# Performance work log

Measured on AMD Instinct MI355X. Metric: run time of the kernel, lower is better.

Reference implementation:

```python
import jax, jax.numpy as jnp
import numpy as np

N_NODES = 100000
N_EDGES = 3200000
D = 256
L = 3
BN_EPS = 1e-5


def setup_inputs() -> dict:
    key = jax.random.key(0)
    ks = jax.random.split(key, 6)
    scale = 1.0 / np.sqrt(D)
    x = jax.random.normal(ks[0], (N_NODES, D), dtype=jnp.float32)
    W = jax.random.normal(ks[1], (L, D, D), dtype=jnp.float32) * scale
    b = jnp.zeros((L, D), dtype=jnp.float32)
    Wl = jax.random.normal(ks[2], (L, D, D), dtype=jnp.float32) * scale
    bl = jnp.zeros((L, D), dtype=jnp.float32)
    gamma = jnp.ones((L, D), dtype=jnp.float32)
    beta = jnp.zeros((L, D), dtype=jnp.float32)
    src = jax.random.randint(ks[3], (N_EDGES,), 0, N_NODES, dtype=jnp.int32)
    dst = jax.random.randint(ks[4], (N_EDGES,), 0, N_NODES, dtype=jnp.int32)
    return {"x": x, "W": W, "b": b, "Wl": Wl, "bl": bl,
            "gamma": gamma, "beta": beta, "src": src, "dst": dst}


def _gcn_head(x, W, b, Wl, bl, gamma, beta, src, dst):
    n = x.shape[0]
    ones = jnp.ones((src.shape[0],), dtype=x.dtype)
    # degrees (clamped to 1, as DGL GraphConv does)
    deg_out = jnp.maximum(jax.ops.segment_sum(ones, src, num_segments=n), 1.0)
    deg_in = jnp.maximum(jax.ops.segment_sum(ones, dst, num_segments=n), 1.0)
    inv_sqrt_out = (deg_out ** -0.5)[:, None]  # [N,1]
    inv_sqrt_in = (deg_in ** -0.5)[:, None]

    h = x
    for l in range(W.shape[0]):
        # GraphConv, norm='both': D_in^{-1/2} A D_out^{-1/2} h W + b
        hs = h * inv_sqrt_out
        agg = jax.ops.segment_sum(hs[src], dst, num_segments=n)  # [N,D]
        agg = agg * inv_sqrt_in
        out = agg @ W[l] + b[l]
        # residual + optional linear on the layer input
        out = out + h + (h @ Wl[l] + bl[l])
        # BatchNorm1d over nodes (training-style batch stats, biased var)
        mean = jnp.mean(out, axis=0)
        var = jnp.var(out, axis=0)
        out = gamma[l] * (out - mean) * jax.lax.rsqrt(var + BN_EPS) + beta[l]
        # ReLU (Dropout treated as identity / eval mode)
        h = jax.nn.relu(out)
    return h


def reference(x, W, b, Wl, bl, gamma, beta, src, dst):
    return _gcn_head(x, W, b, Wl, bl, gamma, beta, src, dst)
```

## Files before the change

kernel.cpp:

```cpp
#include <hip/hip_runtime.h>

#define D 256
#define BN_EPS 1e-5f

typedef __attribute__((ext_vector_type(8))) short short8;
typedef __attribute__((ext_vector_type(4))) float f32x4;
typedef __attribute__((ext_vector_type(2))) float f32x2;

__device__ __forceinline__ float b2f(ushort u) {
    union { unsigned u; float f; } c; c.u = ((unsigned)u) << 16; return c.f;
}
__device__ __forceinline__ ushort f2b(float f) {
    union { float f; unsigned u; } c; c.f = f;
    return (ushort)((c.u + 0x7fffu + ((c.u >> 16) & 1u)) >> 16);
}

typedef __attribute__((address_space(1))) const void gv_t;
typedef __attribute__((address_space(3))) void lv_t;
__device__ __forceinline__ void gld16(const void* g, void* l) {
    __builtin_amdgcn_global_load_lds((gv_t*)g, (lv_t*)l, 16, 0, 0);
}

__device__ __forceinline__ uint2 pk_fp8x8(const float* r) {
    unsigned w0 = 0, w1 = 0;
    w0 = __builtin_amdgcn_cvt_pk_fp8_f32(r[0], r[1], w0, false);
    w0 = __builtin_amdgcn_cvt_pk_fp8_f32(r[2], r[3], w0, true);
    w1 = __builtin_amdgcn_cvt_pk_fp8_f32(r[4], r[5], w1, false);
    w1 = __builtin_amdgcn_cvt_pk_fp8_f32(r[6], r[7], w1, true);
    return make_uint2(w0, w1);
}


#define HB 64

__global__ __launch_bounds__(256) void hist_kernel(const int* __restrict__ src,
                                                   const int* __restrict__ dst,
                                                   unsigned* __restrict__ P, int E) {
    __shared__ unsigned lhist[16384];
    int combo = blockIdx.y;
    const int* arr = (combo >> 2) ? dst : src;
    unsigned base = (unsigned)(combo & 3) << 15;
    for (int j = threadIdx.x; j < 16384; j += 256) lhist[j] = 0;
    __syncthreads();
    int i0 = (blockIdx.x * 256 + threadIdx.x) * 4;
    int stride = HB * 256 * 4;
    for (int i = i0; i < E; i += stride) {
        if (i + 3 < E) {
            int4 v = *(const int4*)(arr + i);
            unsigned r0 = (unsigned)v.x - base;
            unsigned r1 = (unsigned)v.y - base;
            unsigned r2 = (unsigned)v.z - base;
            unsigned r3 = (unsigned)v.w - base;
            if (r0 < 32768u) atomicAdd(&lhist[r0 >> 1], 1u << ((r0 & 1) << 4));
            if (r1 < 32768u) atomicAdd(&lhist[r1 >> 1], 1u << ((r1 & 1) << 4));
            if (r2 < 32768u) atomicAdd(&lhist[r2 >> 1], 1u << ((r2 & 1) << 4));
            if (r3 < 32768u) atomicAdd(&lhist[r3 >> 1], 1u << ((r3 & 1) << 4));
        } else {
            for (int j = i; j < E; j++) {
                unsigned r = (unsigned)arr[j] - base;
                if (r < 32768u) atomicAdd(&lhist[r >> 1], 1u << ((r & 1) << 4));
            }
        }
    }
    __syncthreads();
    unsigned* dstp = P + ((size_t)(combo * HB + blockIdx.x) << 14);
    for (int j = threadIdx.x; j < 16384; j += 256) dstp[j] = lhist[j];
}

__global__ void histreduce_kernel(const unsigned* __restrict__ P,
                                  int* __restrict__ cntO, int* __restrict__ cntI, int N) {
    int g = blockIdx.x * 256 + threadIdx.x;
    int array = g >> 16;
    int p = g & 65535;
    int range = p >> 14;
    int j = p & 16383;
    const unsigned* Pp = P + ((size_t)((array * 4 + range) * HB) << 14) + j;
    unsigned s = 0;
#pragma unroll 8
    for (int b = 0; b < HB; b++) s += Pp[(size_t)b << 14];
    int bin = (range << 15) + 2 * j;
    int* cnt = array ? cntI : cntO;
    if (bin < N)     cnt[bin]     = (int)(s & 0xFFFFu);
    if (bin + 1 < N) cnt[bin + 1] = (int)(s >> 16);
}

__global__ void invsqrt_kernel(const int* __restrict__ cntO, const int* __restrict__ cntI,
                               float* __restrict__ invO, float* __restrict__ invOI,
                               float* __restrict__ sqrtO, int N) {
    int i = blockIdx.x * blockDim.x + threadIdx.x;
    if (i < N) {
        float dO = (float)max(cntO[i], 1);
        float io = rsqrtf(dO);
        invO[i] = io;
        sqrtO[i] = sqrtf(dO);
        invOI[i] = io * rsqrtf((float)max(cntI[i], 1));
    }
}

__global__ void scan1_kernel(const int* __restrict__ cnt, int* __restrict__ off,
                             int* __restrict__ bsum, int n) {
    __shared__ int s[256];
    int t = threadIdx.x;
    int i0 = blockIdx.x * 1024 + t * 4;
    int v0 = (i0 < n) ? ((cnt[i0] + 7) & ~7) : 0;
    int v1 = (i0 + 1 < n) ? ((cnt[i0 + 1] + 7) & ~7) : 0;
    int v2 = (i0 + 2 < n) ? ((cnt[i0 + 2] + 7) & ~7) : 0;
    int v3 = (i0 + 3 < n) ? ((cnt[i0 + 3] + 7) & ~7) : 0;
    int tsum = v0 + v1 + v2 + v3;
    s[t] = tsum;
    __syncthreads();
    for (int d = 1; d < 256; d <<= 1) {
        int x = (t >= d) ? s[t - d] : 0;
        __syncthreads();
        s[t] += x;
        __syncthreads();
    }
    int excl = s[t] - tsum;
    if (i0 < n)     off[i0]     = excl;
    if (i0 + 1 < n) off[i0 + 1] = excl + v0;
    if (i0 + 2 < n) off[i0 + 2] = excl + v0 + v1;
    if (i0 + 3 < n) off[i0 + 3] = excl + v0 + v1 + v2;
    if (t == 255) bsum[blockIdx.x] = s[255];
}

__global__ void scan2_kernel(int* __restrict__ bsum, int nb) {
    __shared__ int s[256];
    int t = threadIdx.x;
    int v = (t < nb) ? bsum[t] : 0;
    s[t] = v;
    __syncthreads();
    for (int d = 1; d < 256; d <<= 1) {
        int x = (t >= d) ? s[t - d] : 0;
        __syncthreads();
        s[t] += x;
        __syncthreads();
    }
    if (t < nb) bsum[t] = s[t] - v;
    if (t == nb - 1) bsum[1023] = s[t];
}

__global__ void scan3_kernel(int* __restrict__ off, const int* __restrict__ bsum,
                             int* __restrict__ bucketCur, int n) {
    int i = blockIdx.x * blockDim.x + threadIdx.x;
    if (i < n) {
        int v = off[i] + bsum[i >> 10];
        off[i] = v;
        if ((i & 255) == 0) bucketCur[i >> 8] = v;
    } else if (i == n) {
        off[n] = bsum[1023];
    }
}


#define NBKMAX 512

__global__ __launch_bounds__(256) void partA_kernel(const int* __restrict__ src,
                                                    const int* __restrict__ dst,
                                                    int* __restrict__ bucketCur,
                                                    unsigned* __restrict__ pairs,
                                                    int E, int NBK) {
    __shared__ int cnt[NBKMAX];
    __shared__ int base_s[NBKMAX];
    for (int j = threadIdx.x; j < NBK; j += 256) cnt[j] = 0;
    __syncthreads();
    for (int i = blockIdx.x * 256 + threadIdx.x; i < E; i += gridDim.x * 256)
        atomicAdd(&cnt[((unsigned)dst[i]) >> 8], 1);
    __syncthreads();
    for (int j = threadIdx.x; j < NBK; j += 256) {
        base_s[j] = atomicAdd(&bucketCur[j], cnt[j]);
        cnt[j] = 0;
    }
    __syncthreads();
    for (int i = blockIdx.x * 256 + threadIdx.x; i < E; i += gridDim.x * 256) {
        unsigned d = (unsigned)dst[i];
        unsigned b = d >> 8;
        int pos = base_s[b] + atomicAdd(&cnt[b], 1);
        pairs[pos] = ((unsigned)src[i] << 8) | (d & 255u);
    }
}

#define BCAP 14336

__global__ __launch_bounds__(256) void partB_kernel(const unsigned* __restrict__ pairs,
                                                    const int* __restrict__ off,
                                                    const int* __restrict__ bucketCur,
                                                    int* __restrict__ srcS, int N) {
    __shared__ int curL[256];
    __shared__ int stage[BCAP];
    int b = blockIdx.x;
    int n0 = b << 8;
    int n1 = min(n0 + 256, N);
    int base = off[n0];
    int len = off[n1] - base;
    if (len > BCAP) len = BCAP;
    for (int j = threadIdx.x; j < len; j += 256) stage[j] = N;
    int nn = n1 - n0;
    for (int i = threadIdx.x; i < nn; i += 256) curL[i] = off[n0 + i] - base;
    __syncthreads();
    int cntB = bucketCur[b] - base;
    for (int j = threadIdx.x; j < cntB; j += 256) {
        unsigned p = pairs[base + j];
        int pos = atomicAdd(&curL[p & 255u], 1);
        if (pos < BCAP) stage[pos] = (int)(p >> 8);
    }
    __syncthreads();
    for (int j4 = threadIdx.x; j4 * 4 < len; j4 += 256)
        *(int4*)(srcS + base + j4 * 4) = *(const int4*)(stage + j4 * 4);
}

__global__ void init_pad_kernel(ushort* __restrict__ X, unsigned* __restrict__ X8,
                                int N, long strideH) {
    int t = threadIdx.x;
    X[(size_t)N * D + t] = 0;
    if (t < 64) X8[(t >> 5) * strideH + (size_t)N * 32 + (t & 31)] = 0;
}


__global__ void prep_w_kernel(const float* __restrict__ W, const float* __restrict__ Wl,
                              const float* __restrict__ b, const float* __restrict__ bl,
                              ushort* __restrict__ Wt, float* __restrict__ bcat, int L) {
    int idx = blockIdx.x * blockDim.x + threadIdx.x;
    int k = idx & 511;
    int n = (idx >> 9) & 255;
    int l = idx >> 17;
    if (l >= L) return;
    float v;
    if (k < 256) {
        v = W[(size_t)l * 65536 + k * 256 + n];
    } else {
        v = Wl[(size_t)l * 65536 + (k - 256) * 256 + n];
        if (k - 256 == n) v += 1.0f;
    }
    Wt[idx] = f2b(v);
    if (k == 0) bcat[l * 256 + n] = b[l * 256 + n] + bl[l * 256 + n];
}

__global__ void x2b_kernel(const float* __restrict__ x, const float* __restrict__ invO,
                           ushort* __restrict__ hs, unsigned* __restrict__ hs8,
                           long strideH, long n8) {
    long i8 = (long)blockIdx.x * blockDim.x + threadIdx.x;
    if (i8 >= n8) return;
    long row = i8 >> 5;
    float sc = invO[row];
    float4 a = ((const float4*)x)[i8 * 2];
    float4 b = ((const float4*)x)[i8 * 2 + 1];
    float r[8] = { a.x * sc, a.y * sc, a.z * sc, a.w * sc,
                   b.x * sc, b.y * sc, b.z * sc, b.w * sc };
    ushort v[8];
#pragma unroll
    for (int j = 0; j < 8; j++) v[j] = f2b(r[j]);
    *(short8*)(hs + i8 * 8) = *(short8*)v;
    long H = (i8 >> 4) & 1;
    *(uint2*)(hs8 + H * strideH + row * 32 + (i8 & 15) * 2) = pk_fp8x8(r);
}


__global__ void aggregate_kernel(const unsigned* __restrict__ hs8h,
                                 const float* __restrict__ invOI,
                                 const int* __restrict__ off, const int* __restrict__ srcS,
                                 ushort* __restrict__ aggsh, int N) {
    int tid = threadIdx.x;
    int wid = tid >> 6, lane = tid & 63;
    int l32 = lane & 31;
    int node = blockIdx.x * 8 + wid * 2 + (lane >> 5);
    if (blockIdx.x * 8 + wid * 2 >= N) return;
    bool valid = node < N;
    int e0 = valid ? off[node] : 0;
    int e1 = valid ? off[node + 1] : 0;
    f32x2 A01 = {0.f, 0.f}, A23 = {0.f, 0.f};
    for (int e = e0; e < e1; e += 8) {
        int4 c0 = *(const int4*)(srcS + e);
        int4 c1 = *(const int4*)(srcS + e + 4);
        unsigned g0 = hs8h[(size_t)c0.x * 32 + l32];
        unsigned g1 = hs8h[(size_t)c0.y * 32 + l32];
        unsigned g2 = hs8h[(size_t)c0.z * 32 + l32];
        unsigned g3 = hs8h[(size_t)c0.w * 32 + l32];
        unsigned g4 = hs8h[(size_t)c1.x * 32 + l32];
        unsigned g5 = hs8h[(size_t)c1.y * 32 + l32];
        unsigned g6 = hs8h[(size_t)c1.z * 32 + l32];
        unsigned g7 = hs8h[(size_t)c1.w * 32 + l32];
#pragma unroll
        for (int q = 0; q < 8; q++) {
            unsigned g = (q == 0) ? g0 : (q == 1) ? g1 : (q == 2) ? g2 : (q == 3) ? g3
                       : (q == 4) ? g4 : (q == 5) ? g5 : (q == 6) ? g6 : g7;
            A01 += __builtin_amdgcn_cvt_pk_f32_fp8(g, false);
            A23 += __builtin_amdgcn_cvt_pk_f32_fp8(g, true);
        }
    }
    if (valid) {
        float wi = invOI[node];
        ushort4 o;
        o.x = f2b(A01[0] * wi); o.y = f2b(A01[1] * wi);
        o.z = f2b(A23[0] * wi); o.w = f2b(A23[1] * wi);
        *(ushort4*)(aggsh + (size_t)node * D + l32 * 4) = o;
    }
}


#define ASOFF(buf) ((buf) * 4096)
#define BSOFF(buf) (8192 + (buf) * 8192)

__global__ __launch_bounds__(512) void gemm_kernel(
        const ushort* __restrict__ aggs, const ushort* __restrict__ hs,
        const ushort* __restrict__ Wt,  const float* __restrict__ bcat,
        const float* __restrict__ sqrtO,
        ushort* __restrict__ tmp, float* __restrict__ bnsum, float* __restrict__ bnsq,
        int M) {
    __shared__ short SH[24576];

    int bm0 = blockIdx.x * 128;
    if (bm0 >= M) return;

    int tid = threadIdx.x;
    int wid = tid >> 6, lane = tid & 63;
    int wr = wid >> 2, wc = wid & 3;
    int lrow = lane & 15, lkh = lane >> 4;
    int srow = lane >> 2;
    int sseg = (lane & 3) ^ ((srow >> 1) & 3);

    f32x4 acc[4][4] = {};

#define STAGE(buf, k0s)                                                                    \
    {                                                                                      \
        int kk_ = (k0s) & 255;                                                             \
        const ushort* Ah_ = ((k0s) < 256) ? aggs : hs;                                     \
        gld16(Ah_ + (size_t)(bm0 + wid * 16 + srow) * 256 + kk_ + sseg * 8,                \
              SH + ASOFF(buf) + (wid * 16) * 32);                                          \
        const ushort* gb_ = Wt + (size_t)(wid * 32 + srow) * 512 + (k0s) + sseg * 8;       \
        gld16(gb_,            SH + BSOFF(buf) + (wid * 32) * 32);                          \
        gld16(gb_ + 16 * 512, SH + BSOFF(buf) + (wid * 32 + 16) * 32);                     \
    }

    STAGE(0, 0);

#pragma unroll
    for (int k0 = 0; k0 < 512; k0 += 32) {
        int cur = (k0 >> 5) & 1;
        __syncthreads();
        if (k0 + 32 < 512) STAGE(cur ^ 1, k0 + 32);

        short8 a[4], bfr[4];
#pragma unroll
        for (int m = 0; m < 4; m++) {
            int ra = wr * 64 + m * 16 + lrow;
            a[m] = *(short8*)&SH[ASOFF(cur) + ra * 32 + (lkh ^ ((ra >> 1) & 3)) * 8];
        }
#pragma unroll
        for (int n = 0; n < 4; n++) {
            int rb = wc * 64 + n * 16 + lrow;
            bfr[n] = *(short8*)&SH[BSOFF(cur) + rb * 32 + (lkh ^ ((rb >> 1) & 3)) * 8];
        }
#pragma unroll
        for (int m = 0; m < 4; m++)
#pragma unroll
            for (int n = 0; n < 4; n++)
                acc[m][n] = __builtin_amdgcn_mfma_f32_16x16x32_bf16(a[m], bfr[n], acc[m][n], 0, 0, 0);
    }
#undef STAGE

    ushort outv[4][4][4];
#pragma unroll
    for (int n = 0; n < 4; n++) {
        int col = wc * 64 + n * 16 + lrow;
        float bc = bcat[col];
        float s_part = 0.f, q_part = 0.f;
#pragma unroll
        for (int m = 0; m < 4; m++) {
            int rbase = bm0 + wr * 64 + m * 16 + lkh * 4;
#pragma unroll
            for (int i = 0; i < 4; i++) {
                int row = rbase + i;
                float v = (row < M) ? (acc[m][n][i] * sqrtO[row] + bc) : 0.f;
                outv[m][n][i] = f2b(v);
                if (row < M) { s_part += v; q_part += v * v; }
            }
        }
        s_part += __shfl_xor(s_part, 16);
        s_part += __shfl_xor(s_part, 32);
        q_part += __shfl_xor(q_part, 16);
        q_part += __shfl_xor(q_part, 32);
        if (lkh == 0) {
            atomicAdd(&bnsum[col], s_part);
            atomicAdd(&bnsq[col], q_part);
        }
    }

    for (int half = 0; half < 2; half++) {
        __syncthreads();
        if (wr == half) {
#pragma unroll
            for (int m = 0; m < 4; m++)
#pragma unroll
                for (int n = 0; n < 4; n++)
#pragma unroll
                    for (int i = 0; i < 4; i++)
                        SH[(m * 16 + lkh * 4 + i) * 256 + wc * 64 + n * 16 + lrow] =
                            (short)outv[m][n][i];
        }
        __syncthreads();
#pragma unroll
        for (int p = 0; p < 4; p++) {
            int rl = (tid >> 5) + p * 16;
            int row = bm0 + half * 64 + rl;
            if (row < M)
                *(short8*)(tmp + (size_t)row * 256 + (tid & 31) * 8) =
                    *(short8*)&SH[rl * 256 + (tid & 31) * 8];
        }
    }
}


__global__ void bnfin_kernel(float* __restrict__ bnsum, float* __restrict__ bnsq,
                             const float* __restrict__ gamma, const float* __restrict__ beta,
                             float2* __restrict__ bnab, float invM) {
    int c = threadIdx.x;
    float mean = bnsum[c] * invM;
    float var = bnsq[c] * invM - mean * mean;
    float a = gamma[c] * rsqrtf(var + BN_EPS);
    bnab[c] = make_float2(a, beta[c] - a * mean);
    bnsum[c] = 0.f;
    bnsq[c] = 0.f;
}

__global__ void bnrelu_kernel(const ushort* __restrict__ tmp, const float2* __restrict__ bnab,
                              const float* __restrict__ invO, ushort* __restrict__ Xout,
                              unsigned* __restrict__ X8out, long strideH,
                              float* __restrict__ out, int M, int last) {
    long i8 = (long)blockIdx.x * blockDim.x + threadIdx.x;
    if (i8 >= (long)M * 32) return;
    long row = i8 >> 5;
    int c0 = ((int)(i8 & 31)) * 8;
    short8 v = *(const short8*)(tmp + row * D + c0);
    float r[8];
#pragma unroll
    for (int j = 0; j < 8; j++) {
        float2 ab = bnab[c0 + j];
        float x = b2f((ushort)v[j]);
        r[j] = fmaxf(ab.x * x + ab.y, 0.f);
    }
    if (last) {
        float4 f0 = make_float4(r[0], r[1], r[2], r[3]);
        float4 f1 = make_float4(r[4], r[5], r[6], r[7]);
        ((float4*)(out + row * D + c0))[0] = f0;
        ((float4*)(out + row * D + c0))[1] = f1;
    } else {
        float sc = invO[row];
        ushort w[8];
#pragma unroll
        for (int j = 0; j < 8; j++) { r[j] *= sc; w[j] = f2b(r[j]); }
        *(short8*)(Xout + row * D + c0) = *(short8*)w;
        long H = (i8 >> 4) & 1;
        *(uint2*)(X8out + H * strideH + row * 32 + (i8 & 15) * 2) = pk_fp8x8(r);
    }
}


extern "C" void kernel_launch(void* const* d_in, const int* in_sizes, int n_in,
                              void* d_out, int out_size, void* d_ws, size_t ws_size,
                              hipStream_t stream) {
    const float* x     = (const float*)d_in[0];
    const float* W     = (const float*)d_in[1];
    const float* b     = (const float*)d_in[2];
    const float* Wl    = (const float*)d_in[3];
    const float* bl    = (const float*)d_in[4];
    const float* gamma = (const float*)d_in[5];
    const float* beta  = (const float*)d_in[6];
    const int*   src   = (const int*)d_in[7];
    const int*   dst   = (const int*)d_in[8];

    const int N = in_sizes[0] / D;
    const int E = in_sizes[7];
    const int L = in_sizes[1] / (D * D);
    const int M_pad = (N + 1 + 127) & ~127;
    const int E_pad = E + 7 * N + 64;
    const int NBK = (N + 255) >> 8;
    const long strideH = (long)M_pad * 32;
    float* out = (float*)d_out;

    char* p = (char*)d_ws;
    auto alloc = [&](size_t bytes) -> char* {
        char* r = p;
        p += (bytes + 255) & ~(size_t)255;
        return r;
    };
    int*      cur   = (int*)alloc((size_t)NBKMAX * 4);
    int*      cntO  = (int*)alloc((size_t)N * 4);
    int*      cntI  = (int*)alloc((size_t)N * 4);
    float*    invO  = (float*)alloc((size_t)(N + 1) * 4);
    float*    invOI = (float*)alloc((size_t)(N + 1) * 4);
    float*    sqrtO = (float*)alloc((size_t)(N + 1) * 4);
    int*      off_  = (int*)alloc((size_t)(N + 1) * 4);
    int*      bsum  = (int*)alloc(1024 * 4);
    int*      srcS  = (int*)alloc((size_t)E_pad * 4);
    ushort*   Wt    = (ushort*)alloc((size_t)L * 256 * 512 * 2);
    float*    bcat  = (float*)alloc((size_t)L * 256 * 4);
    ushort*   X     = (ushort*)alloc((size_t)M_pad * D * 2);
    unsigned* X8    = (unsigned*)alloc((size_t)2 * strideH * 4);
    ushort*   aggs  = (ushort*)alloc((size_t)M_pad * D * 2);
    ushort*   tmp   = (ushort*)alloc((size_t)M_pad * D * 2);
    float*    bnsum = (float*)alloc((size_t)2 * D * 4);
    float*    bnsq  = bnsum + D;
    float2*   bnab  = (float2*)alloc((size_t)D * 8);

    unsigned* P     = (unsigned*)aggs;
    unsigned* pairs = (unsigned*)aggs;

    {
        dim3 hg(HB, 8);
        hist_kernel<<<hg, 256, 0, stream>>>(src, dst, P, E);
        histreduce_kernel<<<512, 256, 0, stream>>>(P, cntO, cntI, N);
    }
    invsqrt_kernel<<<(N + 255) / 256, 256, 0, stream>>>(cntO, cntI, invO, invOI, sqrtO, N);
    int NB = (N + 1023) / 1024;
    scan1_kernel<<<NB, 256, 0, stream>>>(cntI, off_, bsum, N);
    scan2_kernel<<<1, 256, 0, stream>>>(bsum, NB);
    scan3_kernel<<<(N + 256) / 256, 256, 0, stream>>>(off_, bsum, cur, N);
    partA_kernel<<<512, 256, 0, stream>>>(src, dst, cur, pairs, E, NBK);
    partB_kernel<<<NBK, 256, 0, stream>>>(pairs, off_, cur, srcS, N);
    init_pad_kernel<<<1, 256, 0, stream>>>(X, X8, N, strideH);

    prep_w_kernel<<<(L * 256 * 512 + 255) / 256, 256, 0, stream>>>(W, Wl, b, bl, Wt, bcat, L);
    x2b_kernel<<<(int)(((long)N * 32 + 255) / 256), 256, 0, stream>>>(
        x, invO, X, X8, strideH, (long)N * 32);
    hipMemsetAsync(bnsum, 0, 2 * D * sizeof(float), stream);

    const int MB = (N + 127) / 128;
    const int agg_grid = (N + 7) / 8;
    const float invM = 1.0f / (float)N;
    for (int l = 0; l < L; l++) {
        int last = (l == L - 1);

        aggregate_kernel<<<agg_grid, 256, 0, stream>>>(X8, invOI, off_, srcS, aggs, N);
        aggregate_kernel<<<agg_grid, 256, 0, stream>>>(X8 + strideH, invOI, off_, srcS,
                                                       aggs + 128, N);

        gemm_kernel<<<MB, 512, 0, stream>>>(aggs, X, Wt + (size_t)l * 256 * 512,
                                            bcat + l * 256, sqrtO, tmp, bnsum, bnsq, N);

        bnfin_kernel<<<1, 256, 0, stream>>>(bnsum, bnsq, gamma + l * D, beta + l * D, bnab, invM);
        bnrelu_kernel<<<(int)(((long)N * 32 + 255) / 256), 256, 0, stream>>>(
            tmp, bnab, invO, X, X8, strideH, out, N, last);
    }
}
```

Baseline: 764.5 us.

## Single-buffer GEMM LDS to raise occupancy; merge aggregate halves into one launch

The GEMM drops its double-buffered LDS staging for a single buffer, which halves shared memory, and adds a launch-bounds hint so more blocks can be resident per CU. The epilogue now writes its output tile through LDS in four 32-row passes so it fits the smaller buffer. The two per-half aggregate launches become one 2D-grid launch that uses blockIdx.y to pick the half. The trade-off is that load/compute overlap inside a block is lost and each k-step needs an extra barrier, with the hope that higher occupancy hides the latency instead.

```diff
diff --git a/kernel.cpp b/kernel.cpp
--- a/kernel.cpp
+++ b/kernel.cpp
@@ -255,10 +255,12 @@
 }
 
 
-__global__ void aggregate_kernel(const unsigned* __restrict__ hs8h,
+__global__ void aggregate_kernel(const unsigned* __restrict__ X8,
                                  const float* __restrict__ invOI,
                                  const int* __restrict__ off, const int* __restrict__ srcS,
-                                 ushort* __restrict__ aggsh, int N) {
+                                 ushort* __restrict__ aggs, long strideH, int N) {
+    const unsigned* hs8h = X8 + blockIdx.y * strideH;
+    ushort* aggsh = aggs + blockIdx.y * 128;
     int tid = threadIdx.x;
     int wid = tid >> 6, lane = tid & 63;
     int l32 = lane & 31;
@@ -297,16 +299,15 @@
 }
 
 
-#define ASOFF(buf) ((buf) * 4096)
-#define BSOFF(buf) (8192 + (buf) * 8192)
-
-__global__ __launch_bounds__(512) void gemm_kernel(
+#define BSOFF 4096
+
+__global__ __launch_bounds__(512, 8) void gemm_kernel(
         const ushort* __restrict__ aggs, const ushort* __restrict__ hs,
         const ushort* __restrict__ Wt,  const float* __restrict__ bcat,
         const float* __restrict__ sqrtO,
         ushort* __restrict__ tmp, float* __restrict__ bnsum, float* __restrict__ bnsq,
         int M) {
-    __shared__ short SH[24576];
+    __shared__ short SH[12288];
 
     int bm0 = blockIdx.x * 128;
     if (bm0 >= M) return;
@@ -320,43 +321,37 @@
 
     f32x4 acc[4][4] = {};
 
-#define STAGE(buf, k0s)                                                                    \
-    {                                                                                      \
-        int kk_ = (k0s) & 255;                                                             \
-        const ushort* Ah_ = ((k0s) < 256) ? aggs : hs;                                     \
-        gld16(Ah_ + (size_t)(bm0 + wid * 16 + srow) * 256 + kk_ + sseg * 8,                \
-              SH + ASOFF(buf) + (wid * 16) * 32);                                          \
-        const ushort* gb_ = Wt + (size_t)(wid * 32 + srow) * 512 + (k0s) + sseg * 8;       \
-        gld16(gb_,            SH + BSOFF(buf) + (wid * 32) * 32);                          \
-        gld16(gb_ + 16 * 512, SH + BSOFF(buf) + (wid * 32 + 16) * 32);                     \
-    }
-
-    STAGE(0, 0);
-
 #pragma unroll
     for (int k0 = 0; k0 < 512; k0 += 32) {
-        int cur = (k0 >> 5) & 1;
-        __syncthreads();
-        if (k0 + 32 < 512) STAGE(cur ^ 1, k0 + 32);
+        {
+            int kk_ = k0 & 255;
+            const ushort* Ah_ = (k0 < 256) ? aggs : hs;
+            gld16(Ah_ + (size_t)(bm0 + wid * 16 + srow) * 256 + kk_ + sseg * 8,
+                  SH + (wid * 16) * 32);
+            const ushort* gb_ = Wt + (size_t)(wid * 32 + srow) * 512 + k0 + sseg * 8;
+            gld16(gb_,            SH + BSOFF + (wid * 32) * 32);
+            gld16(gb_ + 16 * 512, SH + BSOFF + (wid * 32 + 16) * 32);
+        }
+        __syncthreads();
 
         short8 a[4], bfr[4];
 #pragma unroll
         for (int m = 0; m < 4; m++) {
             int ra = wr * 64 + m * 16 + lrow;
-            a[m] = *(short8*)&SH[ASOFF(cur) + ra * 32 + (lkh ^ ((ra >> 1) & 3)) * 8];
+            a[m] = *(short8*)&SH[ra * 32 + (lkh ^ ((ra >> 1) & 3)) * 8];
         }
 #pragma unroll
         for (int n = 0; n < 4; n++) {
             int rb = wc * 64 + n * 16 + lrow;
-            bfr[n] = *(short8*)&SH[BSOFF(cur) + rb * 32 + (lkh ^ ((rb >> 1) & 3)) * 8];
+            bfr[n] = *(short8*)&SH[BSOFF + rb * 32 + (lkh ^ ((rb >> 1) & 3)) * 8];
         }
 #pragma unroll
         for (int m = 0; m < 4; m++)
 #pragma unroll
             for (int n = 0; n < 4; n++)
                 acc[m][n] = __builtin_amdgcn_mfma_f32_16x16x32_bf16(a[m], bfr[n], acc[m][n], 0, 0, 0);
-    }
-#undef STAGE
+        __syncthreads();
+    }
 
     ushort outv[4][4][4];
 #pragma unroll
@@ -385,26 +380,28 @@
         }
     }
 
-    for (int half = 0; half < 2; half++) {
-        __syncthreads();
-        if (wr == half) {
-#pragma unroll
-            for (int m = 0; m < 4; m++)
+#pragma unroll
+    for (int q = 0; q < 4; q++) {
+        __syncthreads();
+        if (wr == (q >> 1)) {
+#pragma unroll
+            for (int mm = 0; mm < 2; mm++) {
+                int m = (q & 1) * 2 + mm;
 #pragma unroll
                 for (int n = 0; n < 4; n++)
 #pragma unroll
                     for (int i = 0; i < 4; i++)
-                        SH[(m * 16 + lkh * 4 + i) * 256 + wc * 64 + n * 16 + lrow] =
+                        SH[(mm * 16 + lkh * 4 + i) * 256 + wc * 64 + n * 16 + lrow] =
                             (short)outv[m][n][i];
-        }
-        __syncthreads();
-#pragma unroll
-        for (int p = 0; p < 4; p++) {
-            int rl = (tid >> 5) + p * 16;
-            int row = bm0 + half * 64 + rl;
-            if (row < M)
-                *(short8*)(tmp + (size_t)row * 256 + (tid & 31) * 8) =
-                    *(short8*)&SH[rl * 256 + (tid & 31) * 8];
+            }
+        }
+        __syncthreads();
+        int rl = tid >> 4;
+        int c0 = (tid & 15) * 16;
+        int row = bm0 + q * 32 + rl;
+        if (row < M) {
+            *(short8*)(tmp + (size_t)row * 256 + c0)     = *(short8*)&SH[rl * 256 + c0];
+            *(short8*)(tmp + (size_t)row * 256 + c0 + 8) = *(short8*)&SH[rl * 256 + c0 + 8];
         }
     }
 }
@@ -525,14 +522,12 @@
     hipMemsetAsync(bnsum, 0, 2 * D * sizeof(float), stream);
 
     const int MB = (N + 127) / 128;
-    const int agg_grid = (N + 7) / 8;
+    const dim3 ag((N + 7) / 8, 2);
     const float invM = 1.0f / (float)N;
     for (int l = 0; l < L; l++) {
         int last = (l == L - 1);
 
-        aggregate_kernel<<<agg_grid, 256, 0, stream>>>(X8, invOI, off_, srcS, aggs, N);
-        aggregate_kernel<<<agg_grid, 256, 0, stream>>>(X8 + strideH, invOI, off_, srcS,
-                                                       aggs + 128, N);
+        aggregate_kernel<<<ag, 256, 0, stream>>>(X8, invOI, off_, srcS, aggs, strideH, N);
 
         gemm_kernel<<<MB, 512, 0, stream>>>(aggs, X, Wt + (size_t)l * 256 * 512,
                                             bcat + l * 256, sqrtO, tmp, bnsum, bnsq, N);
```

Result: slower. 1.715 ms (+124.3%).
